# Kernel optimization log

Hardware: AMD Instinct MI355X
Metric: run time of the kernel (lower is better)

Reference implementation:

```python
import jax, jax.numpy as jnp
import numpy as np

P = 7  # output_size


def _axis_weights(start, length, dim):
    """Per-roi 1D interpolation matrix A [R, P, dim] such that the roi_align
    output separates as out = Ay @ fm @ Ax^T (torchvision roi_align,
    aligned=False, sampling_ratio=-1 i.e. adaptive ceil(bin) samples)."""
    S = int(np.ceil(dim / P))  # max samples per bin (rois lie inside the image)
    bin_sz = length / P                               # [R]
    grid = jnp.ceil(length / P).astype(jnp.int32)     # adaptive samples per bin, [R]
    g = grid.astype(jnp.float32)[:, None, None]       # [R,1,1]
    s = jnp.arange(S, dtype=jnp.float32)              # [S]
    ph = jnp.arange(P, dtype=jnp.float32)             # [P]
    # sample coordinate: start + ph*bin + (s+0.5)*bin/grid  -> [R,P,S]
    coord = (start[:, None, None] + ph[None, :, None] * bin_sz[:, None, None]
             + (s[None, None, :] + 0.5) * bin_sz[:, None, None] / g)
    valid = (coord >= -1.0) & (coord <= dim)
    c = jnp.maximum(coord, 0.0)
    low = jnp.floor(c).astype(jnp.int32)
    hi_clamp = low >= dim - 1
    low = jnp.where(hi_clamp, dim - 1, low)
    high = jnp.where(hi_clamp, dim - 1, low + 1)
    cv = jnp.where(hi_clamp, low.astype(jnp.float32), c)
    l = cv - low.astype(jnp.float32)
    smask = (s[None, None, :] < g) & valid            # mask unused samples
    w = smask.astype(jnp.float32) / g                 # 1/count split per axis
    w_low = (1.0 - l) * w
    w_high = l * w
    R = start.shape[0]
    r_idx = jnp.arange(R)[:, None, None]
    p_idx = jnp.arange(P)[None, :, None]
    A = jnp.zeros((R, P, dim), dtype=jnp.float32)
    A = A.at[r_idx, p_idx, low].add(w_low)
    A = A.at[r_idx, p_idx, high].add(w_high)
    return A


def _roi_align(fm, rois):
    # fm: [C,H,W]; rois: [R,4] = (x1,y1,x2,y2); spatial_scale=1.0
    C, H, W = fm.shape
    x1, y1, x2, y2 = rois[:, 0], rois[:, 1], rois[:, 2], rois[:, 3]
    roi_w = jnp.maximum(x2 - x1, 1.0)
    roi_h = jnp.maximum(y2 - y1, 1.0)
    Ay = _axis_weights(y1, roi_h, H)                  # [R,P,H]
    Ax = _axis_weights(x1, roi_w, W)                  # [R,P,W]
    tmp = jnp.einsum('rph,chw->rcpw', Ay, fm)         # [R,C,P,W]
    return jnp.einsum('rcpw,rqw->rcpq', tmp, Ax)      # [R,C,P,P]


def _per_image(fm, b, g):
    # fm: [C,H,W], b: [N,4] boxes, g: [M,4] gt boxes
    N, M = b.shape[0], g.shape[0]
    # context boxes: union (min of mins, max of maxes) of every (box, gt) pair
    x1 = jnp.minimum(b[:, None, 0], g[None, :, 0])
    y1 = jnp.minimum(b[:, None, 1], g[None, :, 1])
    x2 = jnp.maximum(b[:, None, 2], g[None, :, 2])
    y2 = jnp.maximum(b[:, None, 3], g[None, :, 3])
    ctx = jnp.stack([x1, y1, x2, y2], axis=-1).reshape(N * M, 4)
    feats = _roi_align(fm, jnp.concatenate([b, ctx], axis=0))  # [N+N*M,C,P,P]
    box_f = feats[:N]
    ctx_mean = feats[N:].reshape(N, M, feats.shape[1], P, P).mean(axis=1)
    return box_f + ctx_mean                            # [N,C,P,P]


def setup_inputs() -> dict:
    key = jax.random.key(0)
    B, C, H, W, N, M = 2, 256, 56, 56, 64, 8
    k1, k2, k3, k4, k5 = jax.random.split(key, 5)
    feature_map = jax.random.normal(k1, (B, C, H, W), dtype=jnp.float32)
    # boxes inside the feature map, max side 0.35*H so adaptive grid <= ceil(H/7)
    b_xy1 = jax.random.uniform(k2, (B, N, 2), minval=0.0, maxval=0.64 * H)
    b_wh = jax.random.uniform(k3, (B, N, 2), minval=4.0, maxval=0.35 * H)
    boxes = jnp.concatenate([b_xy1, b_xy1 + b_wh], axis=-1).astype(jnp.float32)
    g_xy1 = jax.random.uniform(k4, (B, M, 2), minval=0.0, maxval=0.64 * H)
    g_wh = jax.random.uniform(k5, (B, M, 2), minval=4.0, maxval=0.35 * H)
    gt_boxes = jnp.concatenate([g_xy1, g_xy1 + g_wh], axis=-1).astype(jnp.float32)
    return {"feature_map": feature_map, "boxes": boxes, "gt_boxes": gt_boxes}


def reference(feature_map, boxes, gt_boxes):
    # returns [B, N, C, P, P] (stacked version of the per-image list output)
    return jax.vmap(_per_image)(feature_map, boxes, gt_boxes)
```

## Files before the change

kernel.cpp:

```cpp
#include <hip/hip_runtime.h>

#define B_ 2
#define C_ 256
#define H_ 56
#define W_ 56
#define N_ 64
#define M_ 8
#define P_ 7
#define Y2_ (H_/2)
#define Y4_ (H_/4)
#define JR_ (1 + M_)
#define WROW_ 8

typedef _Float16 half2v __attribute__((ext_vector_type(2)));

#if __has_builtin(__builtin_amdgcn_fdot2)
#define FDOT2(a, b, c) __builtin_amdgcn_fdot2((a), (b), (c), false)
#else
static __device__ __forceinline__ float FDOT2(half2v a, half2v b, float c) {
    return fmaf((float)a.x, (float)b.x, fmaf((float)a.y, (float)b.y, c));
}
#endif

#define F_FMT4 0
#define N_FMT4 (B_*Y4_*W_*C_*2)
#define F_OUTS (F_FMT4 + N_FMT4)
#define N_OUTS (B_*N_*49*C_)
#define WS_ELEMS (F_OUTS + N_OUTS)

#define PREP_T (B_*Y4_*4*2)

__global__ __launch_bounds__(256) void k_prep(const float* __restrict__ fm,
                                              float* __restrict__ ws_f) {
    __shared__ float t[28 * 257 + 8];
    int bid = blockIdx.x;
    int tid = (int)threadIdx.x;

    int xh = bid & 1;
    int cg = (bid >> 1) & 3;
    int y4 = (bid >> 3) % Y4_;
    int b  = (bid >> 3) / Y4_;
    int c0 = cg * 64, x0 = xh * 28;
    for (int e = tid; e < 64 * 4 * 28; e += 256) {
        int c_l = e / 112, rem = e % 112;
        int y_l = rem / 28, x_l = rem % 28;
        t[x_l * 257 + y_l * 64 + c_l] =
            fm[(((size_t)b * C_ + c0 + c_l) * H_ + 4 * y4 + y_l) * W_ + x0 + x_l];
    }
    __syncthreads();
    uint2* dst = (uint2*)ws_f;
    for (int e = tid; e < 28 * 64; e += 256) {
        int x_l = e >> 6, c_l = e & 63;
        const float* p = &t[x_l * 257 + c_l];
        half2v lo, hi; uint2 o;
        lo.x = (_Float16)p[0];   lo.y = (_Float16)p[64];
        hi.x = (_Float16)p[128]; hi.y = (_Float16)p[192];
        o.x = __builtin_bit_cast(unsigned int, lo);
        o.y = __builtin_bit_cast(unsigned int, hi);
        dst[(((size_t)b * Y4_ + y4) * W_ + x0 + x_l) * (size_t)C_ + c0 + c_l] = o;
    }
}

__global__ __launch_bounds__(256, 4) void k_main(const float* __restrict__ ws_f,
                                                 const float* __restrict__ boxes,
                                                 const float* __restrict__ gt,
                                                 float* __restrict__ outs) {
    __shared__ float        s_wyf[H_][WROW_];
    __shared__ unsigned int s_wy2[Y2_ * WROW_];
    __shared__ float        s_ax[W_][WROW_];

    int bid = blockIdx.x;
    int k   = bid % JR_;
    int n   = (bid / JR_) & (N_ - 1);
    int b   = bid / (JR_ * N_);
    int tid  = (int)threadIdx.x;
    int c    = tid;

    const float* bp = boxes + ((size_t)b * N_ + n) * 4;
    float bx1, by1, bx2, by2;
    if (k == 0) {
        bx1 = bp[0]; by1 = bp[1]; bx2 = bp[2]; by2 = bp[3];
    } else {
        const float* gp = gt + ((size_t)b * M_ + (k - 1)) * 4;
        bx1 = fminf(bp[0], gp[0]); by1 = fminf(bp[1], gp[1]);
        bx2 = fmaxf(bp[2], gp[2]); by2 = fmaxf(bp[3], gp[3]);
    }
    float rw = fmaxf(bx2 - bx1, 1.0f);
    float rh = fmaxf(by2 - by1, 1.0f);

    for (int e = tid; e < H_ * WROW_; e += 256) ((float*)s_wyf)[e] = 0.0f;
    for (int e = tid; e < W_ * WROW_; e += 256) ((float*)s_ax)[e] = 0.0f;
    __syncthreads();

    if (tid < P_) {
        int p = tid;
        float bin = rh / 7.0f;
        float gf  = ceilf(bin);
        int   g   = (int)gf;
        float ivg = 1.0f / gf;
        float start = by1 + (float)p * bin;
        for (int ss = 0; ss < g; ++ss) {
            float coord = start + ((float)ss + 0.5f) * bin * ivg;
            if (coord < -1.0f || coord > (float)H_) continue;
            float cc = fmaxf(coord, 0.0f);
            int low = (int)floorf(cc);
            int high; float l;
            if (low >= H_ - 1) { low = H_ - 1; high = H_ - 1; l = 0.0f; }
            else               { high = low + 1; l = cc - (float)low; }
            s_wyf[low][p]  += (1.0f - l) * ivg;
            s_wyf[high][p] += l * ivg;
        }
    } else if (tid >= 64 && tid < 64 + P_) {
        int p = tid - 64;
        float bin = rw / 7.0f;
        float gf  = ceilf(bin);
        int   g   = (int)gf;
        float ivg = 1.0f / gf;
        float fs  = (k == 0) ? ivg : ivg * (1.0f / (float)M_);
        float start = bx1 + (float)p * bin;
        for (int ss = 0; ss < g; ++ss) {
            float coord = start + ((float)ss + 0.5f) * bin * ivg;
            if (coord < -1.0f || coord > (float)W_) continue;
            float cc = fmaxf(coord, 0.0f);
            int low = (int)floorf(cc);
            int high; float l;
            if (low >= W_ - 1) { low = W_ - 1; high = W_ - 1; l = 0.0f; }
            else               { high = low + 1; l = cc - (float)low; }
            s_ax[low][p]  += (1.0f - l) * fs;
            s_ax[high][p] += l * fs;
        }
    }
    __syncthreads();

    if (tid < Y2_ * WROW_) {
        int q2 = tid >> 3, col = tid & 7;
        half2v h;
        if (col < P_) { h.x = (_Float16)s_wyf[2 * q2][col]; h.y = (_Float16)s_wyf[2 * q2 + 1][col]; }
        else          { h.x = (_Float16)0.0f; h.y = (_Float16)0.0f; }
        s_wy2[tid] = __builtin_bit_cast(unsigned int, h);
    }
    __syncthreads();

    int xs = min(max((int)floorf(fmaxf(bx1, 0.0f)), 0), W_ - 1);
    int xe = min(max((int)floorf(bx1 + rw) + 1, 0), W_ - 1) + 1;
    int ylo = min(max((int)floorf(fmaxf(by1, 0.0f)), 0), H_ - 1);
    int yhi = min(max((int)floorf(by1 + rh) + 1, 0), H_ - 1) + 1;
    int ylo4 = ylo >> 2;
    int yhi4 = (yhi + 3) >> 2;

    const uint2* f4 = (const uint2*)ws_f + (size_t)b * (Y4_ * W_ * C_);

    float acc[49];
#pragma unroll
    for (int q = 0; q < 49; ++q) acc[q] = 0.0f;
    int live = 0;

    for (int x = xs; x < xe; x += 4) {
        float cs[4][P_];
#pragma unroll
        for (int i = 0; i < 4; ++i)
#pragma unroll
            for (int py = 0; py < P_; ++py) cs[i][py] = 0.0f;

        const uint2* cp = f4 + ((size_t)(ylo4 * W_ + x)) * C_ + c;
        for (int y4 = ylo4; y4 < yhi4; ++y4) {
            uint2 d0 = cp[0];
            uint2 d1 = cp[C_];
            uint2 d2 = cp[2 * C_];
            uint2 d3 = cp[3 * C_];
            uint4 wa0 = *(const uint4*)&s_wy2[(2 * y4) * WROW_];
            uint4 wb0 = *(const uint4*)&s_wy2[(2 * y4) * WROW_ + 4];
            uint4 wa1 = *(const uint4*)&s_wy2[(2 * y4 + 1) * WROW_];
            uint4 wb1 = *(const uint4*)&s_wy2[(2 * y4 + 1) * WROW_ + 4];
            half2v w0[7], w1[7];
            w0[0] = __builtin_bit_cast(half2v, wa0.x);
            w0[1] = __builtin_bit_cast(half2v, wa0.y);
            w0[2] = __builtin_bit_cast(half2v, wa0.z);
            w0[3] = __builtin_bit_cast(half2v, wa0.w);
            w0[4] = __builtin_bit_cast(half2v, wb0.x);
            w0[5] = __builtin_bit_cast(half2v, wb0.y);
            w0[6] = __builtin_bit_cast(half2v, wb0.z);
            w1[0] = __builtin_bit_cast(half2v, wa1.x);
            w1[1] = __builtin_bit_cast(half2v, wa1.y);
            w1[2] = __builtin_bit_cast(half2v, wa1.z);
            w1[3] = __builtin_bit_cast(half2v, wa1.w);
            w1[4] = __builtin_bit_cast(half2v, wb1.x);
            w1[5] = __builtin_bit_cast(half2v, wb1.y);
            w1[6] = __builtin_bit_cast(half2v, wb1.z);
            half2v v0a = __builtin_bit_cast(half2v, d0.x);
            half2v v0b = __builtin_bit_cast(half2v, d0.y);
            half2v v1a = __builtin_bit_cast(half2v, d1.x);
            half2v v1b = __builtin_bit_cast(half2v, d1.y);
            half2v v2a = __builtin_bit_cast(half2v, d2.x);
            half2v v2b = __builtin_bit_cast(half2v, d2.y);
            half2v v3a = __builtin_bit_cast(half2v, d3.x);
            half2v v3b = __builtin_bit_cast(half2v, d3.y);
#pragma unroll
            for (int py = 0; py < P_; ++py) {
                cs[0][py] = FDOT2(w1[py], v0b, FDOT2(w0[py], v0a, cs[0][py]));
                cs[1][py] = FDOT2(w1[py], v1b, FDOT2(w0[py], v1a, cs[1][py]));
                cs[2][py] = FDOT2(w1[py], v2b, FDOT2(w0[py], v2a, cs[2][py]));
                cs[3][py] = FDOT2(w1[py], v3b, FDOT2(w0[py], v3a, cs[3][py]));
            }
            cp += W_ * C_;
        }

#pragma unroll
        for (int i = 0; i < 4; ++i) {
            if (x + i < xe) {
                float av[8];
                *(float4*)(&av[0]) = *(const float4*)&s_ax[x + i][0];
                *(float4*)(&av[4]) = *(const float4*)&s_ax[x + i][4];
#pragma unroll
                for (int px = 0; px < P_; ++px) {
                    float w = av[px];
                    if (w != 0.0f) {
                        live |= 1 << px;
#pragma unroll
                        for (int py = 0; py < P_; ++py)
                            acc[py * P_ + px] = fmaf(w, cs[i][py], acc[py * P_ + px]);
                    }
                }
            }
        }
    }

    float* os = outs + ((size_t)b * N_ + n) * (49 * C_) + c;
#pragma unroll
    for (int px = 0; px < P_; ++px) {
        if (live & (1 << px)) {
#pragma unroll
            for (int py = 0; py < P_; ++py)
                atomicAdd(os + (py * P_ + px) * C_, acc[py * P_ + px]);
        }
    }
}

__global__ __launch_bounds__(256) void k_final(const float* __restrict__ outs,
                                               float* __restrict__ out) {
    __shared__ float t[49 * 65];
    int bid = blockIdx.x;
    int cg  = bid & 3;
    int bn  = bid >> 2;
    int tid = (int)threadIdx.x;
    const float* src = outs + (size_t)bn * (49 * C_) + cg * 64;
    for (int e = tid; e < 49 * 64; e += 256) {
        int q = e >> 6, c = e & 63;
        t[q * 65 + c] = src[q * C_ + c];
    }
    __syncthreads();
    float* dst = out + (size_t)bn * (C_ * 49) + (size_t)cg * 64 * 49;
    for (int e = tid; e < 64 * 49; e += 256) {
        int c = e / 49, q = e - c * 49;
        dst[e] = t[q * 65 + c];
    }
}

extern "C" void kernel_launch(void* const* d_in, const int* in_sizes, int n_in,
                              void* d_out, int out_size, void* d_ws, size_t ws_size,
                              hipStream_t stream) {
    const float* fm    = (const float*)d_in[0];
    const float* boxes = (const float*)d_in[1];
    const float* gt    = (const float*)d_in[2];
    float* ws_f = (float*)d_ws;
    float* out  = (float*)d_out;
    float* outs = ws_f + F_OUTS;

    hipMemsetAsync(outs, 0, (size_t)N_OUTS * sizeof(float), stream);
    k_prep<<<PREP_T, 256, 0, stream>>>(fm, ws_f);
    k_main<<<B_ * N_ * JR_, 256, 0, stream>>>(ws_f, boxes, gt, outs);
    k_final<<<B_ * N_ * 4, 256, 0, stream>>>(outs, out);
}
```

Baseline: 157.7 us.

## Split roi_align work across output column pairs and fold memset into prep kernel

Each (box, context) block is split into four blocks, each covering two output columns px and only the x range those columns need. This cuts the accumulator from 49 to 14 registers, so launch bounds can rise to 8 waves. The y-weighted column sums are now recomputed per x instead of batched over four x columns. The output zeroing memset moves into extra blocks of the prep kernel, removing one launch. The trade is more blocks and some repeated feature loads and y-dot work across the four column slices.

```diff
diff --git a/kernel.cpp b/kernel.cpp
--- a/kernel.cpp
+++ b/kernel.cpp
@@ -9,7 +9,8 @@
 #define P_ 7
 #define Y2_ (H_/2)
 #define Y4_ (H_/4)
-#define JR_ (1 + M_)
+#define KR_ (1 + M_)
+#define JPB_ (KR_*4)
 #define WROW_ 8
 
 typedef _Float16 half2v __attribute__((ext_vector_type(2)));
@@ -29,6 +30,7 @@
 #define WS_ELEMS (F_OUTS + N_OUTS)
 
 #define PREP_T (B_*Y4_*4*2)
+#define PREP_N (PREP_T + 784)
 
 __global__ __launch_bounds__(256) void k_prep(const float* __restrict__ fm,
                                               float* __restrict__ ws_f) {
@@ -36,32 +38,43 @@
     int bid = blockIdx.x;
     int tid = (int)threadIdx.x;
 
-    int xh = bid & 1;
-    int cg = (bid >> 1) & 3;
-    int y4 = (bid >> 3) % Y4_;
-    int b  = (bid >> 3) / Y4_;
-    int c0 = cg * 64, x0 = xh * 28;
-    for (int e = tid; e < 64 * 4 * 28; e += 256) {
-        int c_l = e / 112, rem = e % 112;
-        int y_l = rem / 28, x_l = rem % 28;
-        t[x_l * 257 + y_l * 64 + c_l] =
-            fm[(((size_t)b * C_ + c0 + c_l) * H_ + 4 * y4 + y_l) * W_ + x0 + x_l];
-    }
-    __syncthreads();
-    uint2* dst = (uint2*)ws_f;
-    for (int e = tid; e < 28 * 64; e += 256) {
-        int x_l = e >> 6, c_l = e & 63;
-        const float* p = &t[x_l * 257 + c_l];
-        half2v lo, hi; uint2 o;
-        lo.x = (_Float16)p[0];   lo.y = (_Float16)p[64];
-        hi.x = (_Float16)p[128]; hi.y = (_Float16)p[192];
-        o.x = __builtin_bit_cast(unsigned int, lo);
-        o.y = __builtin_bit_cast(unsigned int, hi);
-        dst[(((size_t)b * Y4_ + y4) * W_ + x0 + x_l) * (size_t)C_ + c0 + c_l] = o;
-    }
-}
-
-__global__ __launch_bounds__(256, 4) void k_main(const float* __restrict__ ws_f,
+    if (bid < PREP_T) {
+        int xh = bid & 1;
+        int cg = (bid >> 1) & 3;
+        int y4 = (bid >> 3) % Y4_;
+        int b  = (bid >> 3) / Y4_;
+        int c0 = cg * 64, x0 = xh * 28;
+        for (int e = tid; e < 64 * 4 * 28; e += 256) {
+            int c_l = e / 112, rem = e % 112;
+            int y_l = rem / 28, x_l = rem % 28;
+            t[x_l * 257 + y_l * 64 + c_l] =
+                fm[(((size_t)b * C_ + c0 + c_l) * H_ + 4 * y4 + y_l) * W_ + x0 + x_l];
+        }
+        __syncthreads();
+        uint2* dst = (uint2*)ws_f;
+        for (int e = tid; e < 28 * 64; e += 256) {
+            int x_l = e >> 6, c_l = e & 63;
+            const float* p = &t[x_l * 257 + c_l];
+            half2v lo, hi; uint2 o;
+            lo.x = (_Float16)p[0];   lo.y = (_Float16)p[64];
+            hi.x = (_Float16)p[128]; hi.y = (_Float16)p[192];
+            o.x = __builtin_bit_cast(unsigned int, lo);
+            o.y = __builtin_bit_cast(unsigned int, hi);
+            dst[(((size_t)b * Y4_ + y4) * W_ + x0 + x_l) * (size_t)C_ + c0 + c_l] = o;
+        }
+        return;
+    }
+
+    {
+        int tz = (bid - PREP_T) * 256 + tid;
+        float4 z = {0.0f, 0.0f, 0.0f, 0.0f};
+        float4* dst = (float4*)(ws_f + F_OUTS);
+        dst[tz * 2]     = z;
+        dst[tz * 2 + 1] = z;
+    }
+}
+
+__global__ __launch_bounds__(256, 8) void k_main(const float* __restrict__ ws_f,
                                                  const float* __restrict__ boxes,
                                                  const float* __restrict__ gt,
                                                  float* __restrict__ outs) {
@@ -70,11 +83,14 @@
     __shared__ float        s_ax[W_][WROW_];
 
     int bid = blockIdx.x;
-    int k   = bid % JR_;
-    int n   = (bid / JR_) & (N_ - 1);
-    int b   = bid / (JR_ * N_);
-    int tid  = (int)threadIdx.x;
-    int c    = tid;
+    int j   = bid % JPB_;
+    int n   = (bid / JPB_) & (N_ - 1);
+    int b   = bid / (JPB_ * N_);
+    int k   = j >> 2;
+    int s   = j & 3;
+    int p0  = 2 * s;
+    int tid = (int)threadIdx.x;
+    int c   = tid;
 
     const float* bp = boxes + ((size_t)b * N_ + n) * 4;
     float bx1, by1, bx2, by2;
@@ -141,8 +157,14 @@
     }
     __syncthreads();
 
-    int xs = min(max((int)floorf(fmaxf(bx1, 0.0f)), 0), W_ - 1);
-    int xe = min(max((int)floorf(bx1 + rw) + 1, 0), W_ - 1) + 1;
+    float binw = rw * (1.0f / 7.0f);
+    float lo_f = bx1 + (float)p0 * binw;
+    int   pe   = (p0 + 1 < P_) ? p0 + 2 : p0 + 1;
+    float hi_f = bx1 + (float)pe * binw;
+    int xs = min(max((int)floorf(fmaxf(lo_f, 0.0f)), 0), W_ - 1);
+    int xe = min(max((int)floorf(fminf(hi_f, (float)W_)) + 1, 0), W_ - 1) + 1;
+    if (xs >= xe) return;
+
     int ylo = min(max((int)floorf(fmaxf(by1, 0.0f)), 0), H_ - 1);
     int yhi = min(max((int)floorf(by1 + rh) + 1, 0), H_ - 1) + 1;
     int ylo4 = ylo >> 2;
@@ -150,89 +172,58 @@
 
     const uint2* f4 = (const uint2*)ws_f + (size_t)b * (Y4_ * W_ * C_);
 
-    float acc[49];
-#pragma unroll
-    for (int q = 0; q < 49; ++q) acc[q] = 0.0f;
-    int live = 0;
-
-    for (int x = xs; x < xe; x += 4) {
-        float cs[4][P_];
-#pragma unroll
-        for (int i = 0; i < 4; ++i)
-#pragma unroll
-            for (int py = 0; py < P_; ++py) cs[i][py] = 0.0f;
-
-        const uint2* cp = f4 + ((size_t)(ylo4 * W_ + x)) * C_ + c;
-        for (int y4 = ylo4; y4 < yhi4; ++y4) {
-            uint2 d0 = cp[0];
-            uint2 d1 = cp[C_];
-            uint2 d2 = cp[2 * C_];
-            uint2 d3 = cp[3 * C_];
-            uint4 wa0 = *(const uint4*)&s_wy2[(2 * y4) * WROW_];
-            uint4 wb0 = *(const uint4*)&s_wy2[(2 * y4) * WROW_ + 4];
-            uint4 wa1 = *(const uint4*)&s_wy2[(2 * y4 + 1) * WROW_];
-            uint4 wb1 = *(const uint4*)&s_wy2[(2 * y4 + 1) * WROW_ + 4];
-            half2v w0[7], w1[7];
-            w0[0] = __builtin_bit_cast(half2v, wa0.x);
-            w0[1] = __builtin_bit_cast(half2v, wa0.y);
-            w0[2] = __builtin_bit_cast(half2v, wa0.z);
-            w0[3] = __builtin_bit_cast(half2v, wa0.w);
-            w0[4] = __builtin_bit_cast(half2v, wb0.x);
-            w0[5] = __builtin_bit_cast(half2v, wb0.y);
-            w0[6] = __builtin_bit_cast(half2v, wb0.z);
-            w1[0] = __builtin_bit_cast(half2v, wa1.x);
-            w1[1] = __builtin_bit_cast(half2v, wa1.y);
-            w1[2] = __builtin_bit_cast(half2v, wa1.z);
-            w1[3] = __builtin_bit_cast(half2v, wa1.w);
-            w1[4] = __builtin_bit_cast(half2v, wb1.x);
-            w1[5] = __builtin_bit_cast(half2v, wb1.y);
-            w1[6] = __builtin_bit_cast(half2v, wb1.z);
-            half2v v0a = __builtin_bit_cast(half2v, d0.x);
-            half2v v0b = __builtin_bit_cast(half2v, d0.y);
-            half2v v1a = __builtin_bit_cast(half2v, d1.x);
-            half2v v1b = __builtin_bit_cast(half2v, d1.y);
-            half2v v2a = __builtin_bit_cast(half2v, d2.x);
-            half2v v2b = __builtin_bit_cast(half2v, d2.y);
-            half2v v3a = __builtin_bit_cast(half2v, d3.x);
-            half2v v3b = __builtin_bit_cast(half2v, d3.y);
+    float acc0[P_], acc1[P_];
+#pragma unroll
+    for (int q = 0; q < P_; ++q) { acc0[q] = 0.0f; acc1[q] = 0.0f; }
+
+    for (int y4 = ylo4; y4 < yhi4; ++y4) {
+        uint4 wa = *(const uint4*)&s_wy2[(2 * y4) * WROW_];
+        uint4 wb = *(const uint4*)&s_wy2[(2 * y4) * WROW_ + 4];
+        uint4 wc = *(const uint4*)&s_wy2[(2 * y4 + 1) * WROW_];
+        uint4 wd = *(const uint4*)&s_wy2[(2 * y4 + 1) * WROW_ + 4];
+        half2v wlo[7], whi[7];
+        wlo[0] = __builtin_bit_cast(half2v, wa.x);
+        wlo[1] = __builtin_bit_cast(half2v, wa.y);
+        wlo[2] = __builtin_bit_cast(half2v, wa.z);
+        wlo[3] = __builtin_bit_cast(half2v, wa.w);
+        wlo[4] = __builtin_bit_cast(half2v, wb.x);
+        wlo[5] = __builtin_bit_cast(half2v, wb.y);
+        wlo[6] = __builtin_bit_cast(half2v, wb.z);
+        whi[0] = __builtin_bit_cast(half2v, wc.x);
+        whi[1] = __builtin_bit_cast(half2v, wc.y);
+        whi[2] = __builtin_bit_cast(half2v, wc.z);
+        whi[3] = __builtin_bit_cast(half2v, wc.w);
+        whi[4] = __builtin_bit_cast(half2v, wd.x);
+        whi[5] = __builtin_bit_cast(half2v, wd.y);
+        whi[6] = __builtin_bit_cast(half2v, wd.z);
+
+        const uint2* cp = f4 + ((size_t)(y4 * W_ + xs)) * C_ + c;
+        for (int x = xs; x < xe; ++x) {
+            uint2 d = *cp;
+            cp += C_;
+            float2 axv = *(const float2*)&s_ax[x][p0];
+            half2v va = __builtin_bit_cast(half2v, d.x);
+            half2v vb = __builtin_bit_cast(half2v, d.y);
+            float t[P_];
+#pragma unroll
+            for (int py = 0; py < P_; ++py)
+                t[py] = FDOT2(whi[py], vb, FDOT2(wlo[py], va, 0.0f));
 #pragma unroll
             for (int py = 0; py < P_; ++py) {
-                cs[0][py] = FDOT2(w1[py], v0b, FDOT2(w0[py], v0a, cs[0][py]));
-                cs[1][py] = FDOT2(w1[py], v1b, FDOT2(w0[py], v1a, cs[1][py]));
-                cs[2][py] = FDOT2(w1[py], v2b, FDOT2(w0[py], v2a, cs[2][py]));
-                cs[3][py] = FDOT2(w1[py], v3b, FDOT2(w0[py], v3a, cs[3][py]));
+                acc0[py] = fmaf(axv.x, t[py], acc0[py]);
+                acc1[py] = fmaf(axv.y, t[py], acc1[py]);
             }
-            cp += W_ * C_;
-        }
-
-#pragma unroll
-        for (int i = 0; i < 4; ++i) {
-            if (x + i < xe) {
-                float av[8];
-                *(float4*)(&av[0]) = *(const float4*)&s_ax[x + i][0];
-                *(float4*)(&av[4]) = *(const float4*)&s_ax[x + i][4];
-#pragma unroll
-                for (int px = 0; px < P_; ++px) {
-                    float w = av[px];
-                    if (w != 0.0f) {
-                        live |= 1 << px;
-#pragma unroll
-                        for (int py = 0; py < P_; ++py)
-                            acc[py * P_ + px] = fmaf(w, cs[i][py], acc[py * P_ + px]);
-                    }
-                }
-            }
         }
     }
 
     float* os = outs + ((size_t)b * N_ + n) * (49 * C_) + c;
 #pragma unroll
-    for (int px = 0; px < P_; ++px) {
-        if (live & (1 << px)) {
-#pragma unroll
-            for (int py = 0; py < P_; ++py)
-                atomicAdd(os + (py * P_ + px) * C_, acc[py * P_ + px]);
-        }
+    for (int py = 0; py < P_; ++py)
+        atomicAdd(os + (py * P_ + p0) * C_, acc0[py]);
+    if (p0 + 1 < P_) {
+#pragma unroll
+        for (int py = 0; py < P_; ++py)
+            atomicAdd(os + (py * P_ + p0 + 1) * C_, acc1[py]);
     }
 }
 
@@ -266,8 +257,7 @@
     float* out  = (float*)d_out;
     float* outs = ws_f + F_OUTS;
 
-    hipMemsetAsync(outs, 0, (size_t)N_OUTS * sizeof(float), stream);
-    k_prep<<<PREP_T, 256, 0, stream>>>(fm, ws_f);
-    k_main<<<B_ * N_ * JR_, 256, 0, stream>>>(ws_f, boxes, gt, outs);
+    k_prep<<<PREP_N, 256, 0, stream>>>(fm, ws_f);
+    k_main<<<B_ * N_ * JPB_, 256, 0, stream>>>(ws_f, boxes, gt, outs);
     k_final<<<B_ * N_ * 4, 256, 0, stream>>>(outs, out);
 }
```

After: 182.3 us. +15.6%, slower.
